# Optimization experiments

Measured on AMD Instinct MI355X. Metric: run time of the kernel, lower is better.

## Reference

```python
import jax, jax.numpy as jnp
import numpy as np

LSTM_IN = 125
LSTM_H = 125
MLP_D_H = 512
N = 512


def _lstm_scan(x, Wih, Whh, bih, bhh):
    # x: (N, LSTM_IN); PyTorch gate order: i, f, g, o
    H = LSTM_H
    def step(carry, xt):
        h, c = carry
        g = Wih @ xt + Whh @ h + bih + bhh  # (4H,)
        i = jax.nn.sigmoid(g[:H])
        f = jax.nn.sigmoid(g[H:2 * H])
        gg = jnp.tanh(g[2 * H:3 * H])
        o = jax.nn.sigmoid(g[3 * H:])
        c = f * c + i * gg
        h = o * jnp.tanh(c)
        return (h, c), h
    init = (jnp.zeros((H,), x.dtype), jnp.zeros((H,), x.dtype))
    _, hs = jax.lax.scan(step, init, x)
    return hs  # (N, H)


def setup_inputs() -> dict:
    key = jax.random.key(0)
    ks = jax.random.split(key, 14)
    s = 0.05
    d = {
        "sentence_emb": jax.random.normal(ks[0], (N, 1, LSTM_IN), jnp.float32),
        "Wih_f": jax.random.normal(ks[1], (4 * LSTM_H, LSTM_IN), jnp.float32) * s,
        "Whh_f": jax.random.normal(ks[2], (4 * LSTM_H, LSTM_H), jnp.float32) * s,
        "bih_f": jax.random.normal(ks[3], (4 * LSTM_H,), jnp.float32) * s,
        "bhh_f": jax.random.normal(ks[4], (4 * LSTM_H,), jnp.float32) * s,
        "Wih_b": jax.random.normal(ks[5], (4 * LSTM_H, LSTM_IN), jnp.float32) * s,
        "Whh_b": jax.random.normal(ks[6], (4 * LSTM_H, LSTM_H), jnp.float32) * s,
        "bih_b": jax.random.normal(ks[7], (4 * LSTM_H,), jnp.float32) * s,
        "bhh_b": jax.random.normal(ks[8], (4 * LSTM_H,), jnp.float32) * s,
        "W1": jax.random.normal(ks[9], (MLP_D_H, 4 * LSTM_H), jnp.float32) * s,
        "b1": jax.random.normal(ks[10], (MLP_D_H,), jnp.float32) * s,
        "W2": jax.random.normal(ks[11], (1, MLP_D_H), jnp.float32) * s,
        "b2": jax.random.normal(ks[12], (1,), jnp.float32) * s,
    }
    return d


def reference(sentence_emb, Wih_f, Whh_f, bih_f, bhh_f, Wih_b, Whh_b, bih_b, bhh_b, W1, b1, W2, b2):
    x = sentence_emb[:, 0, :]  # (N, 125), batch=1
    h_fwd = _lstm_scan(x, Wih_f, Whh_f, bih_f, bhh_f)           # (N, 125)
    h_bwd = _lstm_scan(x[::-1], Wih_b, Whh_b, bih_b, bhh_b)[::-1]  # (N, 125)
    h = jnp.concatenate([h_fwd, h_bwd], axis=-1)  # (N, 250)
    # output_mtx[i, j] = MLP(concat(h[j], h[i]))
    # Decompose first linear: W1 @ cat(h_j, h_i) = Wa @ h_j + Wb @ h_i
    D = h.shape[-1]
    Pa = h @ W1[:, :D].T   # (N, H): contribution of h_j
    Pb = h @ W1[:, D:].T   # (N, H): contribution of h_i
    hidden = jnp.tanh(Pb[:, None, :] + Pa[None, :, :] + b1)  # (N, N, H)
    out = hidden @ W2[0] + b2[0]  # (N, N)
    return out
```

## Files before the change

### kernel.cpp

```cpp
#include <hip/hip_runtime.h>

typedef __bf16 bf16_t;
typedef __bf16 bf16x8 __attribute__((ext_vector_type(8)));
typedef float f32x4 __attribute__((ext_vector_type(4)));
typedef int   int4v __attribute__((ext_vector_type(4)));

#define LOG2E 1.4426950408889634f

template<int CTRL>
__device__ __forceinline__ float qperm(float x) {
  return __builtin_bit_cast(float,
      __builtin_amdgcn_update_dpp(0, __builtin_bit_cast(int, x), CTRL, 0xF, 0xF, true));
}

__device__ __forceinline__ void lds_barrier() {
  asm volatile("s_waitcnt lgkmcnt(0)\n\ts_barrier" ::: "memory");
}

__global__ __launch_bounds__(256) void pre_kernel(
    const float* __restrict__ x,
    const float* __restrict__ Wih_f, const float* __restrict__ bih_f,
    const float* __restrict__ bhh_f,
    const float* __restrict__ Wih_b, const float* __restrict__ bih_b,
    const float* __restrict__ bhh_b,
    float* __restrict__ preT)
{
  const int dir = blockIdx.x >> 5;
  const int T   = blockIdx.x & 31;
  const float* __restrict__ Wih = dir ? Wih_b : Wih_f;
  const float* __restrict__ bih = dir ? bih_b : bih_f;
  const float* __restrict__ bhh = dir ? bhh_b : bhh_f;

  const int tid = threadIdx.x;
  const int wv  = tid >> 6;
  const int lane = tid & 63;
  const int q = lane >> 4, cc = lane & 15;

  const int r  = 16 * T + cc;
  const int na = r >> 2, pa = r & 3;
  const bool vld = (na < 125);
  const float* __restrict__ Wr = Wih + (vld ? (125 * pa + na) * 125 : 0);

  bf16x8 whi[4], wlo[4];
  #pragma unroll
  for (int ks = 0; ks < 4; ++ks) {
    #pragma unroll
    for (int j = 0; j < 8; ++j) {
      int k = 32 * ks + 8 * q + j;
      float wvv = (vld && k < 125) ? Wr[k] : 0.0f;
      bf16_t hi = (bf16_t)wvv;
      whi[ks][j] = hi;
      wlo[ks][j] = (bf16_t)(wvv - (float)hi);
    }
  }

  float bias[4];
  #pragma unroll
  for (int reg = 0; reg < 4; ++reg) {
    int ro = 16 * T + 4 * q + reg;
    int no = ro >> 2, po = ro & 3;
    bias[reg] = (no < 125) ? (bih[125 * po + no] + bhh[125 * po + no]) : 0.0f;
  }

  for (int i = 0; i < 8; ++i) {
    const int tt = 8 * wv + i;
    const int t  = 16 * tt + cc;
    const int trow = dir ? (511 - t) : t;
    const float* __restrict__ xr = x + trow * 125;

    f32x4 acc = (f32x4)0.0f;
    #pragma unroll
    for (int ks = 0; ks < 4; ++ks) {
      bf16x8 xhi, xlo;
      #pragma unroll
      for (int j = 0; j < 8; ++j) {
        int k = 32 * ks + 8 * q + j;
        float xv = (k < 125) ? xr[k] : 0.0f;
        bf16_t hi = (bf16_t)xv;
        xhi[j] = hi;
        xlo[j] = (bf16_t)(xv - (float)hi);
      }
      acc = __builtin_amdgcn_mfma_f32_16x16x32_bf16(whi[ks], xhi, acc, 0, 0, 0);
      acc = __builtin_amdgcn_mfma_f32_16x16x32_bf16(whi[ks], xlo, acc, 0, 0, 0);
      acc = __builtin_amdgcn_mfma_f32_16x16x32_bf16(wlo[ks], xhi, acc, 0, 0, 0);
    }
    #pragma unroll
    for (int reg = 0; reg < 4; ++reg) {
      int ro = 16 * T + 4 * q + reg;
      preT[dir * 262144 + ro * 512 + 16 * tt + cc] = acc[reg] + bias[reg];
    }
  }
}

__global__ __launch_bounds__(1024, 4) void lstm_kernel(
    const float* __restrict__ Whh_f, const float* __restrict__ Whh_b,
    const float* __restrict__ pre,
    bf16_t* __restrict__ h_all)
{
  const int dir = blockIdx.x;
  const float* __restrict__ Whh = dir ? Whh_b : Whh_f;

  const int tid  = threadIdx.x;
  const int lane = tid & 63;
  const int w    = tid >> 6;
  const int q    = lane >> 4;
  const int cc   = lane & 15;
  const int lt   = cc >> 2;
  const int p    = cc & 3;
  const int ltp  = lt & 1;

  float wm = 0.0f;
  #pragma unroll
  for (int LT = 0; LT < 2; ++LT) {
    int rr = 16 * (2 * w + LT) + cc;
    int nn = rr >> 2, pp = rr & 3;
    if (nn < 125) {
      const float* __restrict__ Wrow = Whh + (125 * pp + nn) * 125;
      #pragma unroll
      for (int ks = 0; ks < 2; ++ks)
        #pragma unroll
        for (int jj = 0; jj < 16; ++jj) {
          int k = 64 * ks + 16 * q + jj;
          if (k < 125) wm = fmaxf(wm, fabsf(Wrow[k]));
        }
    }
  }
  #pragma unroll
  for (int off = 1; off < 64; off <<= 1)
    wm = fmaxf(wm, __shfl_xor(wm, off));
  __shared__ float wmx[16];
  if (lane == 0) wmx[w] = wm;
  __syncthreads();
  float wmax = wmx[0];
  #pragma unroll
  for (int u = 1; u < 16; ++u) wmax = fmaxf(wmax, wmx[u]);
  const float s_w  = 127.0f / wmax;
  const float invq = wmax / (127.0f * 127.0f);

  int4v afrag[2][2];
  #pragma unroll
  for (int LT = 0; LT < 2; ++LT) {
    int rr = 16 * (2 * w + LT) + cc;
    int nn = rr >> 2, pp = rr & 3;
    bool avld = (nn < 125);
    const float* __restrict__ Wrow = Whh + (avld ? (125 * pp + nn) * 125 : 0);
    #pragma unroll
    for (int ks = 0; ks < 2; ++ks) {
      int4v v;
      #pragma unroll
      for (int word = 0; word < 4; ++word) {
        int b = 0;
        #pragma unroll
        for (int byte = 0; byte < 4; ++byte) {
          int jj = 4 * word + byte;
          int k  = 64 * ks + 16 * q + jj;
          int qv = 0;
          if (avld && k < 125)
            qv = (int)__builtin_rintf(Wrow[k] * s_w);
          b |= (qv & 0xFF) << (8 * byte);
        }
        v[word] = b;
      }
      afrag[LT][ks] = v;
    }
  }

  __shared__ __align__(16) char hbuf[2][128];
  if (tid < 256) hbuf[tid >> 7][tid & 127] = 0;
  if (dir == 0 && tid < 512) {
    #pragma unroll
    for (int u = 0; u < 6; ++u)
      h_all[tid * 256 + 250 + u] = (bf16_t)0.0f;
  }
  __syncthreads();

  const int   r_lane = 32 * w + 16 * ltp + 4 * q + p;
  const int   n0     = 8 * w + 4 * ltp + q;
  const float mult   = (p == 2) ? (-2.0f * LOG2E) : (-LOG2E);
  const float sA     = (p == 2) ? 2.0f : 1.0f;
  const float sB     = (p == 2) ? -1.0f : 0.0f;
  const float dscale = mult * invq;
  const float* __restrict__ preR = pre + dir * 262144 + r_lane * 512;
  float c = 0.0f;

  float4 pv_cur = *(const float4*)preR;

  for (int g = 0; g < 128; ++g) {
    float4 pv_nxt = make_float4(0.f, 0.f, 0.f, 0.f);
    if (g < 127) pv_nxt = *(const float4*)(preR + 4 * (g + 1));

    #pragma unroll
    for (int s4 = 0; s4 < 4; ++s4) {
      const int step = 4 * g + s4;
      const int cur  = s4 & 1, nxt = cur ^ 1;
      const float pv = (s4 == 0) ? pv_cur.x : (s4 == 1) ? pv_cur.y
                     : (s4 == 2) ? pv_cur.z : pv_cur.w;
      const float pvm = mult * pv;

      int4v b0 = *(const int4v*)&hbuf[cur][16 * q];
      int4v b1 = *(const int4v*)&hbuf[cur][64 + 16 * q];

      int4v a0 = (int4v)0;
      a0 = __builtin_amdgcn_mfma_i32_16x16x64_i8(afrag[0][0], b0, a0, 0, 0, 0);
      a0 = __builtin_amdgcn_mfma_i32_16x16x64_i8(afrag[0][1], b1, a0, 0, 0, 0);
      int4v a1 = (int4v)0;
      a1 = __builtin_amdgcn_mfma_i32_16x16x64_i8(afrag[1][0], b0, a1, 0, 0, 0);
      a1 = __builtin_amdgcn_mfma_i32_16x16x64_i8(afrag[1][1], b1, a1, 0, 0, 0);

      int4v vA;
      #pragma unroll
      for (int i = 0; i < 4; ++i) vA[i] = ltp ? a1[i] : a0[i];
      int a01 = (p & 1) ? vA[1] : vA[0];
      int a23 = (p & 1) ? vA[3] : vA[2];
      int gsel = (p & 2) ? a23 : a01;

      float xg  = fmaf((float)gsel, dscale, pvm);
      float e   = __builtin_amdgcn_exp2f(xg);
      float y   = __builtin_amdgcn_rcpf(1.0f + e);
      float act = fmaf(y, sA, sB);

      float b_i = qperm<0x00>(act);
      float b_f = qperm<0x55>(act);
      float b_g = qperm<0xAA>(act);
      float b_o = qperm<0xFF>(act);
      c = fmaf(b_f, c, b_i * b_g);
      float e2 = __builtin_amdgcn_exp2f(-2.0f * LOG2E * c);
      float tc = fmaf(__builtin_amdgcn_rcpf(1.0f + e2), 2.0f, -1.0f);
      float h  = b_o * tc;

      if (p == 0 && lt < 2) {
        hbuf[nxt][n0] = (char)(int)__builtin_rintf(h * 127.0f);
        if (n0 < 125) {
          int t_orig = dir ? (511 - step) : step;
          h_all[t_orig * 256 + dir * 125 + n0] = (bf16_t)h;
        }
      }
      lds_barrier();
    }
    pv_cur = pv_nxt;
  }
}

__global__ __launch_bounds__(256) void qgemm_kernel(
    const bf16_t* __restrict__ h_all,
    const float* __restrict__ W1,
    const float* __restrict__ b1,
    float* __restrict__ Qa,
    float* __restrict__ Qb)
{
  const int tid  = threadIdx.x;
  const int wv   = tid >> 6;
  const int lane = tid & 63;
  const int q    = lane >> 4, cc = lane & 15;
  const int bj   = blockIdx.x & 31;
  const int bm   = blockIdx.x >> 5;
  const int m    = bm * 64 + wv * 16 + cc;
  const int j0   = bj * 16;
  const int jA   = j0 + cc;

  const bool isB = (m >= 512);
  const int  row = isB ? (m - 512) : m;
  const int  cof = isB ? 250 : 0;

  f32x4 acc = (f32x4)0.0f;
  #pragma unroll
  for (int ks = 0; ks < 8; ++ks) {
    int kb = 32 * ks + 8 * q;
    bf16x8 a = *(const bf16x8*)&h_all[jA * 256 + kb];
    bf16x8 b;
    #pragma unroll
    for (int jj = 0; jj < 8; ++jj) {
      int k = kb + jj;
      float v = (k < 250) ? W1[row * 500 + cof + k] : 0.0f;
      b[jj] = (bf16_t)v;
    }
    acc = __builtin_amdgcn_mfma_f32_16x16x32_bf16(a, b, acc, 0, 0, 0);
  }

  const float C2 = 2.0f * LOG2E;
  #pragma unroll
  for (int reg = 0; reg < 4; ++reg) {
    int j = j0 + 4 * q + reg;
    float v = acc[reg];
    if (!isB) Qa[j * 512 + m] = C2 * v;
    else      Qb[j * 512 + (m - 512)] = C2 * (v + b1[m - 512]);
  }
}

__global__ __launch_bounds__(256) void outer_kernel(
    const float* __restrict__ Qa, const float* __restrict__ Qb,
    const float* __restrict__ W2, const float* __restrict__ b2,
    float* __restrict__ out)
{
  __shared__ float sa[2][32][33];
  __shared__ float sb[2][32][33];
  __shared__ float sw[2][32];

  const int tid  = threadIdx.x;
  const int bk   = blockIdx.x >> 8;
  const int tile = blockIdx.x & 255;
  const int bi   = tile >> 4, bjx = tile & 15;
  const int i0   = bi * 32, j0 = bjx * 32;
  const int ii0  = (tid & 15) * 2;
  const int jj0  = (tid >> 4) * 2;
  const int ljj  = tid & 31, kk4 = (tid >> 5) * 4;
  const int kbase = bk * 256;

  float accR[2][2] = {{0.0f, 0.0f}, {0.0f, 0.0f}};
  float wsum = 0.0f;

  for (int kc = 0; kc < 8; ++kc) {
    const int buf = kc & 1;
    const int k0  = kbase + kc * 32;
    float4 va = *(const float4*)&Qa[(j0 + ljj) * 512 + k0 + kk4];
    float4 vb = *(const float4*)&Qb[(i0 + ljj) * 512 + k0 + kk4];
    sa[buf][kk4 + 0][ljj] = va.x; sa[buf][kk4 + 1][ljj] = va.y;
    sa[buf][kk4 + 2][ljj] = va.z; sa[buf][kk4 + 3][ljj] = va.w;
    sb[buf][kk4 + 0][ljj] = vb.x; sb[buf][kk4 + 1][ljj] = vb.y;
    sb[buf][kk4 + 2][ljj] = vb.z; sb[buf][kk4 + 3][ljj] = vb.w;
    if (tid < 32) sw[buf][tid] = W2[k0 + tid];
    __syncthreads();

    #pragma unroll 4
    for (int kk = 0; kk < 32; ++kk) {
      float2 av = *(const float2*)&sa[buf][kk][jj0];
      float2 bv = *(const float2*)&sb[buf][kk][ii0];
      float wk = sw[buf][kk];
      wsum += wk;
      {
        float e = __builtin_amdgcn_exp2f(av.x + bv.x);
        accR[0][0] = fmaf(wk, __builtin_amdgcn_rcpf(1.0f + e), accR[0][0]);
      }
      {
        float e = __builtin_amdgcn_exp2f(av.y + bv.x);
        accR[0][1] = fmaf(wk, __builtin_amdgcn_rcpf(1.0f + e), accR[0][1]);
      }
      {
        float e = __builtin_amdgcn_exp2f(av.x + bv.y);
        accR[1][0] = fmaf(wk, __builtin_amdgcn_rcpf(1.0f + e), accR[1][0]);
      }
      {
        float e = __builtin_amdgcn_exp2f(av.y + bv.y);
        accR[1][1] = fmaf(wk, __builtin_amdgcn_rcpf(1.0f + e), accR[1][1]);
      }
    }
  }

  const float bb = (bk == 0) ? b2[0] : 0.0f;
  #pragma unroll
  for (int i2 = 0; i2 < 2; ++i2)
    #pragma unroll
    for (int j2 = 0; j2 < 2; ++j2)
      atomicAdd(&out[(i0 + ii0 + i2) * 512 + (j0 + jj0 + j2)],
                wsum - 2.0f * accR[i2][j2] + bb);
}

extern "C" void kernel_launch(void* const* d_in, const int* in_sizes, int n_in,
                              void* d_out, int out_size, void* d_ws, size_t ws_size,
                              hipStream_t stream) {
  const float* emb   = (const float*)d_in[0];
  const float* Wih_f = (const float*)d_in[1];
  const float* Whh_f = (const float*)d_in[2];
  const float* bih_f = (const float*)d_in[3];
  const float* bhh_f = (const float*)d_in[4];
  const float* Wih_b = (const float*)d_in[5];
  const float* Whh_b = (const float*)d_in[6];
  const float* bih_b = (const float*)d_in[7];
  const float* bhh_b = (const float*)d_in[8];
  const float* W1    = (const float*)d_in[9];
  const float* b1    = (const float*)d_in[10];
  const float* W2    = (const float*)d_in[11];
  const float* b2    = (const float*)d_in[12];
  float* out = (float*)d_out;

  char* ws = (char*)d_ws;
  float*  pre   = (float*)ws;
  bf16_t* h_all = (bf16_t*)(ws + 2 * 1024 * 1024);
  float*  Qa    = (float*)(ws + 2 * 1024 * 1024 + 256 * 1024);
  float*  Qb    = Qa + 512 * 512;

  pre_kernel<<<64, 256, 0, stream>>>(emb, Wih_f, bih_f, bhh_f,
                                     Wih_b, bih_b, bhh_b, pre);
  lstm_kernel<<<2, 1024, 0, stream>>>(Whh_f, Whh_b, pre, h_all);
  qgemm_kernel<<<512, 256, 0, stream>>>(h_all, W1, b1, Qa, Qb);
  hipMemsetAsync(out, 0, (size_t)out_size * sizeof(float), stream);
  outer_kernel<<<512, 256, 0, stream>>>(Qa, Qb, W2, b2, out);
}
```

Measured before the change: 355.8 us.

## Replace LSTM recurrent MFMA with per-thread sdot4 dot products in half-size block

The recurrent hidden-state matvec in the LSTM kernel switches from int8 MFMA tiles across 16 waves to per-thread packed int8 sdot4 dot products. Each quad of threads covers one hidden unit, each thread takes a 32-wide slice of K, and partial sums are reduced across the quad with DPP permutes. The block shrinks from 1024 to 512 threads, so fewer waves take part in each per-step barrier. In exchange each thread does more serial dot-product work per step and holds 32 weight registers.

```diff
diff --git a/kernel.cpp b/kernel.cpp
--- a/kernel.cpp
+++ b/kernel.cpp
@@ -11,6 +11,10 @@
 __device__ __forceinline__ float qperm(float x) {
   return __builtin_bit_cast(float,
       __builtin_amdgcn_update_dpp(0, __builtin_bit_cast(int, x), CTRL, 0xF, 0xF, true));
+}
+template<int CTRL>
+__device__ __forceinline__ int qpermi(int x) {
+  return __builtin_amdgcn_update_dpp(0, x, CTRL, 0xF, 0xF, true);
 }
 
 __device__ __forceinline__ void lds_barrier() {
@@ -92,7 +96,7 @@
   }
 }
 
-__global__ __launch_bounds__(1024, 4) void lstm_kernel(
+__global__ __launch_bounds__(512, 2) void lstm_kernel(
     const float* __restrict__ Whh_f, const float* __restrict__ Whh_b,
     const float* __restrict__ pre,
     bf16_t* __restrict__ h_all)
@@ -100,119 +104,110 @@
   const int dir = blockIdx.x;
   const float* __restrict__ Whh = dir ? Whh_b : Whh_f;
 
-  const int tid  = threadIdx.x;
-  const int lane = tid & 63;
-  const int w    = tid >> 6;
-  const int q    = lane >> 4;
-  const int cc   = lane & 15;
-  const int lt   = cc >> 2;
-  const int p    = cc & 3;
-  const int ltp  = lt & 1;
+  const int tid = threadIdx.x;
+  const int w   = tid >> 6;
+  const int p   = tid & 3;
+  const int Q   = tid >> 2;
+  const bool valid = (Q < 125);
 
   float wm = 0.0f;
-  #pragma unroll
-  for (int LT = 0; LT < 2; ++LT) {
-    int rr = 16 * (2 * w + LT) + cc;
-    int nn = rr >> 2, pp = rr & 3;
-    if (nn < 125) {
-      const float* __restrict__ Wrow = Whh + (125 * pp + nn) * 125;
-      #pragma unroll
-      for (int ks = 0; ks < 2; ++ks)
-        #pragma unroll
-        for (int jj = 0; jj < 16; ++jj) {
-          int k = 64 * ks + 16 * q + jj;
-          if (k < 125) wm = fmaxf(wm, fabsf(Wrow[k]));
-        }
+  if (valid) {
+    #pragma unroll
+    for (int g = 0; g < 4; ++g) {
+      const float* __restrict__ Wrow = Whh + (125 * g + Q) * 125;
+      #pragma unroll
+      for (int kk = 0; kk < 32; ++kk) {
+        int k = 32 * p + kk;
+        if (k < 125) wm = fmaxf(wm, fabsf(Wrow[k]));
+      }
     }
   }
   #pragma unroll
   for (int off = 1; off < 64; off <<= 1)
     wm = fmaxf(wm, __shfl_xor(wm, off));
-  __shared__ float wmx[16];
-  if (lane == 0) wmx[w] = wm;
+  __shared__ float wmx[8];
+  if ((tid & 63) == 0) wmx[w] = wm;
   __syncthreads();
   float wmax = wmx[0];
   #pragma unroll
-  for (int u = 1; u < 16; ++u) wmax = fmaxf(wmax, wmx[u]);
+  for (int u = 1; u < 8; ++u) wmax = fmaxf(wmax, wmx[u]);
   const float s_w  = 127.0f / wmax;
   const float invq = wmax / (127.0f * 127.0f);
 
-  int4v afrag[2][2];
-  #pragma unroll
-  for (int LT = 0; LT < 2; ++LT) {
-    int rr = 16 * (2 * w + LT) + cc;
-    int nn = rr >> 2, pp = rr & 3;
-    bool avld = (nn < 125);
-    const float* __restrict__ Wrow = Whh + (avld ? (125 * pp + nn) * 125 : 0);
-    #pragma unroll
-    for (int ks = 0; ks < 2; ++ks) {
-      int4v v;
-      #pragma unroll
-      for (int word = 0; word < 4; ++word) {
-        int b = 0;
-        #pragma unroll
-        for (int byte = 0; byte < 4; ++byte) {
-          int jj = 4 * word + byte;
-          int k  = 64 * ks + 16 * q + jj;
-          int qv = 0;
-          if (avld && k < 125)
-            qv = (int)__builtin_rintf(Wrow[k] * s_w);
-          b |= (qv & 0xFF) << (8 * byte);
-        }
-        v[word] = b;
-      }
-      afrag[LT][ks] = v;
+  int wq[4][8];
+  #pragma unroll
+  for (int g = 0; g < 4; ++g) {
+    const float* __restrict__ Wrow = Whh + (valid ? (125 * g + Q) * 125 : 0);
+    #pragma unroll
+    for (int d = 0; d < 8; ++d) {
+      int b = 0;
+      #pragma unroll
+      for (int byte = 0; byte < 4; ++byte) {
+        int k = 32 * p + 4 * d + byte;
+        int qv = 0;
+        if (valid && k < 125)
+          qv = (int)__builtin_rintf(Wrow[k] * s_w);
+        b |= (qv & 0xFF) << (8 * byte);
+      }
+      wq[g][d] = b;
     }
   }
 
   __shared__ __align__(16) char hbuf[2][128];
   if (tid < 256) hbuf[tid >> 7][tid & 127] = 0;
-  if (dir == 0 && tid < 512) {
-    #pragma unroll
-    for (int u = 0; u < 6; ++u)
-      h_all[tid * 256 + 250 + u] = (bf16_t)0.0f;
+  if (dir == 0) {
+    #pragma unroll
+    for (int u = 0; u < 6; ++u) h_all[tid * 256 + 250 + u] = (bf16_t)0.0f;
   }
   __syncthreads();
 
-  const int   r_lane = 32 * w + 16 * ltp + 4 * q + p;
-  const int   n0     = 8 * w + 4 * ltp + q;
   const float mult   = (p == 2) ? (-2.0f * LOG2E) : (-LOG2E);
   const float sA     = (p == 2) ? 2.0f : 1.0f;
   const float sB     = (p == 2) ? -1.0f : 0.0f;
   const float dscale = mult * invq;
-  const float* __restrict__ preR = pre + dir * 262144 + r_lane * 512;
+  const float* __restrict__ preR = pre + dir * 262144 + tid * 512;
   float c = 0.0f;
 
   float4 pv_cur = *(const float4*)preR;
 
-  for (int g = 0; g < 128; ++g) {
+  for (int gg = 0; gg < 128; ++gg) {
     float4 pv_nxt = make_float4(0.f, 0.f, 0.f, 0.f);
-    if (g < 127) pv_nxt = *(const float4*)(preR + 4 * (g + 1));
+    if (gg < 127) pv_nxt = *(const float4*)(preR + 4 * (gg + 1));
 
     #pragma unroll
     for (int s4 = 0; s4 < 4; ++s4) {
-      const int step = 4 * g + s4;
+      const int step = 4 * gg + s4;
       const int cur  = s4 & 1, nxt = cur ^ 1;
       const float pv = (s4 == 0) ? pv_cur.x : (s4 == 1) ? pv_cur.y
                      : (s4 == 2) ? pv_cur.z : pv_cur.w;
       const float pvm = mult * pv;
 
-      int4v b0 = *(const int4v*)&hbuf[cur][16 * q];
-      int4v b1 = *(const int4v*)&hbuf[cur][64 + 16 * q];
-
-      int4v a0 = (int4v)0;
-      a0 = __builtin_amdgcn_mfma_i32_16x16x64_i8(afrag[0][0], b0, a0, 0, 0, 0);
-      a0 = __builtin_amdgcn_mfma_i32_16x16x64_i8(afrag[0][1], b1, a0, 0, 0, 0);
-      int4v a1 = (int4v)0;
-      a1 = __builtin_amdgcn_mfma_i32_16x16x64_i8(afrag[1][0], b0, a1, 0, 0, 0);
-      a1 = __builtin_amdgcn_mfma_i32_16x16x64_i8(afrag[1][1], b1, a1, 0, 0, 0);
-
-      int4v vA;
-      #pragma unroll
-      for (int i = 0; i < 4; ++i) vA[i] = ltp ? a1[i] : a0[i];
-      int a01 = (p & 1) ? vA[1] : vA[0];
-      int a23 = (p & 1) ? vA[3] : vA[2];
-      int gsel = (p & 2) ? a23 : a01;
+      const int4v hv0 = *(const int4v*)&hbuf[cur][32 * p];
+      const int4v hv1 = *(const int4v*)&hbuf[cur][32 * p + 16];
+
+      int acc[4];
+      #pragma unroll
+      for (int g = 0; g < 4; ++g) {
+        int a = 0;
+        a = __builtin_amdgcn_sdot4(wq[g][0], hv0[0], a, false);
+        a = __builtin_amdgcn_sdot4(wq[g][1], hv0[1], a, false);
+        a = __builtin_amdgcn_sdot4(wq[g][2], hv0[2], a, false);
+        a = __builtin_amdgcn_sdot4(wq[g][3], hv0[3], a, false);
+        a = __builtin_amdgcn_sdot4(wq[g][4], hv1[0], a, false);
+        a = __builtin_amdgcn_sdot4(wq[g][5], hv1[1], a, false);
+        a = __builtin_amdgcn_sdot4(wq[g][6], hv1[2], a, false);
+        a = __builtin_amdgcn_sdot4(wq[g][7], hv1[3], a, false);
+        acc[g] = a;
+      }
+
+      #pragma unroll
+      for (int g = 0; g < 4; ++g) {
+        int s1 = acc[g] + qpermi<0xB1>(acc[g]);
+        acc[g] = s1 + qpermi<0x4E>(s1);
+      }
+      int g01  = (p & 1) ? acc[1] : acc[0];
+      int g23  = (p & 1) ? acc[3] : acc[2];
+      int gsel = (p & 2) ? g23 : g01;
 
       float xg  = fmaf((float)gsel, dscale, pvm);
       float e   = __builtin_amdgcn_exp2f(xg);
@@ -228,11 +223,11 @@
       float tc = fmaf(__builtin_amdgcn_rcpf(1.0f + e2), 2.0f, -1.0f);
       float h  = b_o * tc;
 
-      if (p == 0 && lt < 2) {
-        hbuf[nxt][n0] = (char)(int)__builtin_rintf(h * 127.0f);
-        if (n0 < 125) {
+      if (p == 0) {
+        hbuf[nxt][Q] = (char)(int)__builtin_rintf(h * 127.0f);
+        if (Q < 125) {
           int t_orig = dir ? (511 - step) : step;
-          h_all[t_orig * 256 + dir * 125 + n0] = (bf16_t)h;
+          h_all[t_orig * 256 + dir * 125 + Q] = (bf16_t)h;
         }
       }
       lds_barrier();
@@ -381,7 +376,7 @@
 
   pre_kernel<<<64, 256, 0, stream>>>(emb, Wih_f, bih_f, bhh_f,
                                      Wih_b, bih_b, bhh_b, pre);
-  lstm_kernel<<<2, 1024, 0, stream>>>(Whh_f, Whh_b, pre, h_all);
+  lstm_kernel<<<2, 512, 0, stream>>>(Whh_f, Whh_b, pre, h_all);
   qgemm_kernel<<<512, 256, 0, stream>>>(h_all, W1, b1, Qa, Qb);
   hipMemsetAsync(out, 0, (size_t)out_size * sizeof(float), stream);
   outer_kernel<<<512, 256, 0, stream>>>(Qa, Qb, W2, b2, out);
```

Measured after the change: 363.3 us. 2.1% more time.
